# Performance work log

Hardware: AMD Instinct MI355X
Metric: run time of the kernel (lower is better)

The kernel has to match this reference:

```python
import jax, jax.numpy as jnp
import numpy as np

OBJ_THRESHOLD = 0.5  # matches module init kwarg
N, M, S = 128, 32, 512


def setup_inputs() -> dict:
    key = jax.random.key(0)
    k = jax.random.split(key, 6)
    # boxes are normalized cxcywh in [0,1]; keep them inside the image so
    # torch-style slice semantics (non-negative indices) are reproduced exactly
    p_cxy = jax.random.uniform(k[0], (N, M, 2), minval=0.3, maxval=0.7)
    p_wh = jax.random.uniform(k[1], (N, M, 2), minval=0.05, maxval=0.4)
    p_cls = jnp.zeros((N, M, 1), jnp.float32)  # C=1 -> all class 0
    p_obj = jax.random.uniform(k[2], (N, M, 1))
    pred_boxes = jnp.concatenate([p_cxy, p_wh, p_cls, p_obj], axis=-1)  # [N,M,6]
    t_cxy = jax.random.uniform(k[3], (N, M, 2), minval=0.3, maxval=0.7)
    t_wh = jax.random.uniform(k[4], (N, M, 2), minval=0.05, maxval=0.4)
    t_cls = jnp.zeros((N, M, 1), jnp.float32)
    target_boxes = jnp.concatenate([t_cxy, t_wh, t_cls], axis=-1)  # [N,M,5]
    return {"pred_boxes": pred_boxes, "target_boxes": target_boxes, "img_size": S}


def _rasterize(boxes, valid, img_size):
    # boxes: [N, M, >=4] normalized cxcywh; valid: [N, M] bool
    # Returns per-sample union-of-boxes mask [N, H, W] (C=1, cls ignored).
    b = img_size * jax.lax.stop_gradient(boxes[..., :4])
    cx, cy, w, h = b[..., 0], b[..., 1], b[..., 2], b[..., 3]
    # torch: .int() truncation (== trunc/floor for positive), then clamp_max(img_size)
    x1 = jnp.minimum((cx - w / 2).astype(jnp.int32), img_size)
    x2 = jnp.minimum((cx + w / 2).astype(jnp.int32), img_size)
    y1 = jnp.minimum((cy - h / 2).astype(jnp.int32), img_size)
    y2 = jnp.minimum((cy + h / 2).astype(jnp.int32), img_size)
    coords = jnp.arange(img_size, dtype=jnp.int32)
    ym = (coords >= y1[..., None]) & (coords < y2[..., None]) & valid[..., None]  # [N,M,H]
    xm = (coords >= x1[..., None]) & (coords < x2[..., None]) & valid[..., None]  # [N,M,W]
    # union over the M boxes without materializing [N,M,H,W]:
    cnt = jnp.einsum('nmh,nmw->nhw', ym.astype(jnp.float32), xm.astype(jnp.float32))
    return cnt > 0  # [N,H,W] bool


def reference(pred_boxes, target_boxes, img_size):
    pred_valid = pred_boxes[..., 5] > OBJ_THRESHOLD          # filter_obj_threshold
    tgt_valid = jnp.ones(target_boxes.shape[:2], dtype=bool)  # all targets valid
    m1 = _rasterize(pred_boxes, pred_valid, img_size)
    m2 = _rasterize(target_boxes, tgt_valid, img_size)
    intersection = (m1 & m2).astype(jnp.float32).sum()  # sum over (N,H,W), C=1
    union = (m1 | m2).astype(jnp.float32).sum()
    return intersection / jnp.maximum(union, 1.0)  # compute(): IoU scalar
```

## Files before the change

### kernel.cpp

```cpp
#include <hip/hip_runtime.h>


#define MAX_M 32
#define MAX_W 8

__global__ void box_mask_iou_kernel(const float* __restrict__ pred,
                                    const float* __restrict__ tgt,
                                    const int* __restrict__ img_size_p,
                                    unsigned int* __restrict__ counters,
                                    int M) {
    const int n   = blockIdx.x;
    const int S   = img_size_p[0];
    const int W   = (S + 63) >> 6;
    const int tid = threadIdx.x;

    __shared__ unsigned long long pmask[MAX_M][MAX_W];
    __shared__ unsigned long long tmask[MAX_M][MAX_W];
    __shared__ int py1[MAX_M], py2[MAX_M], ty1[MAX_M], ty2[MAX_M];

    if (tid < 2 * M) {
        const bool isPred = tid < M;
        const int  m      = isPred ? tid : tid - M;
        const float* b    = isPred ? (pred + (size_t)(n * M + m) * 6)
                                   : (tgt  + (size_t)(n * M + m) * 5);
        const float cx = (float)S * b[0];
        const float cy = (float)S * b[1];
        const float w  = (float)S * b[2];
        const float h  = (float)S * b[3];
        const bool valid = isPred ? (b[5] > 0.5f) : true;
        int x1 = min((int)(cx - w * 0.5f), S);
        int x2 = min((int)(cx + w * 0.5f), S);
        int y1 = min((int)(cy - h * 0.5f), S);
        int y2 = min((int)(cy + h * 0.5f), S);
        if (!valid) { x1 = 0; x2 = 0; y1 = 0; y2 = 0; }
        x1 = max(x1, 0);
        x2 = max(x2, 0);
        unsigned long long (*mask)[MAX_W] = isPred ? pmask : tmask;
        for (int j = 0; j < W; ++j) {
            const int lo = max(x1, j * 64);
            const int hi = min(x2, j * 64 + 64);
            unsigned long long mw = 0ull;
            if (hi > lo) {
                const int len = hi - lo;
                mw = (len >= 64) ? ~0ull : ((1ull << len) - 1ull);
                mw <<= (lo - j * 64);
            }
            mask[m][j] = mw;
        }
        if (isPred) { py1[m] = y1; py2[m] = y2; }
        else        { ty1[m] = y1; ty2[m] = y2; }
    }
    __syncthreads();

    unsigned int localI = 0, localU = 0;
    const int y = blockIdx.y * blockDim.x + tid;
    if (y < S) {
        unsigned long long pm[MAX_W], tm[MAX_W];
        #pragma unroll
        for (int j = 0; j < MAX_W; ++j) { pm[j] = 0ull; tm[j] = 0ull; }
        for (int m = 0; m < M; ++m) {
            if (y >= py1[m] && y < py2[m]) {
                for (int j = 0; j < W; ++j) pm[j] |= pmask[m][j];
            }
            if (y >= ty1[m] && y < ty2[m]) {
                for (int j = 0; j < W; ++j) tm[j] |= tmask[m][j];
            }
        }
        for (int j = 0; j < W; ++j) {
            localI += (unsigned int)__popcll(pm[j] & tm[j]);
            localU += (unsigned int)__popcll(pm[j] | tm[j]);
        }
    }

    #pragma unroll
    for (int off = 32; off > 0; off >>= 1) {
        localI += __shfl_down(localI, off);
        localU += __shfl_down(localU, off);
    }
    if ((tid & 63) == 0) {
        atomicAdd(&counters[0], localI);
        atomicAdd(&counters[1], localU);
    }
}

__global__ void finalize_kernel(const unsigned int* __restrict__ counters,
                                float* __restrict__ out) {
    const double I = (double)counters[0];
    const double U = (double)counters[1];
    out[0] = (float)(I / (U < 1.0 ? 1.0 : U));
}

extern "C" void kernel_launch(void* const* d_in, const int* in_sizes, int n_in,
                              void* d_out, int out_size, void* d_ws, size_t ws_size,
                              hipStream_t stream) {
    const float* pred  = (const float*)d_in[0];
    const float* tgt   = (const float*)d_in[1];
    const int*   imgsz = (const int*)d_in[2];
    float*       out   = (float*)d_out;

    const int M = 32;
    const int N = in_sizes[0] / (6 * M);

    unsigned int* counters = (unsigned int*)d_ws;
    hipMemsetAsync(counters, 0, 2 * sizeof(unsigned int), stream);

    dim3 grid(N, 2);
    box_mask_iou_kernel<<<grid, 256, 0, stream>>>(pred, tgt, imgsz, counters, M);
    finalize_kernel<<<1, 1, 0, stream>>>(counters, out);
}
```

Before: 41.08 us.

## Replace global atomics and memset with per-block partials and parallel finalize

Drops the memset and the global atomicAdd counters. Each block (one per sample, now 512 threads covering all rows) reduces its wave sums through shared memory and writes its own partial pair, and a 64-thread finalize kernel sums the partials with shuffles. This removes a memset launch, atomic contention and the duplicate per-sample box setup across two y-blocks. The cost is fewer blocks (128 instead of 256) and an extra shared-memory barrier.

```diff
diff --git a/kernel.cpp b/kernel.cpp
--- a/kernel.cpp
+++ b/kernel.cpp
@@ -1,28 +1,29 @@
 #include <hip/hip_runtime.h>
 
 
-#define MAX_M 32
+#define MBOX  32
 #define MAX_W 8
 
-__global__ void box_mask_iou_kernel(const float* __restrict__ pred,
-                                    const float* __restrict__ tgt,
-                                    const int* __restrict__ img_size_p,
-                                    unsigned int* __restrict__ counters,
-                                    int M) {
+__global__ __launch_bounds__(512)
+void box_mask_partial_kernel(const float* __restrict__ pred,
+                             const float* __restrict__ tgt,
+                             const int* __restrict__ img_size_p,
+                             unsigned int* __restrict__ partials) {
     const int n   = blockIdx.x;
     const int S   = img_size_p[0];
     const int W   = (S + 63) >> 6;
     const int tid = threadIdx.x;
 
-    __shared__ unsigned long long pmask[MAX_M][MAX_W];
-    __shared__ unsigned long long tmask[MAX_M][MAX_W];
-    __shared__ int py1[MAX_M], py2[MAX_M], ty1[MAX_M], ty2[MAX_M];
+    __shared__ unsigned long long pmask[MBOX][MAX_W];
+    __shared__ unsigned long long tmask[MBOX][MAX_W];
+    __shared__ int py1[MBOX], py2[MBOX], ty1[MBOX], ty2[MBOX];
+    __shared__ unsigned int waveI[8], waveU[8];
 
-    if (tid < 2 * M) {
-        const bool isPred = tid < M;
-        const int  m      = isPred ? tid : tid - M;
-        const float* b    = isPred ? (pred + (size_t)(n * M + m) * 6)
-                                   : (tgt  + (size_t)(n * M + m) * 5);
+    if (tid < 2 * MBOX) {
+        const bool isPred = tid < MBOX;
+        const int  m      = isPred ? tid : tid - MBOX;
+        const float* b    = isPred ? (pred + (size_t)(n * MBOX + m) * 6)
+                                   : (tgt  + (size_t)(n * MBOX + m) * 5);
         const float cx = (float)S * b[0];
         const float cy = (float)S * b[1];
         const float w  = (float)S * b[2];
@@ -53,12 +54,11 @@
     __syncthreads();
 
     unsigned int localI = 0, localU = 0;
-    const int y = blockIdx.y * blockDim.x + tid;
-    if (y < S) {
+    for (int y = tid; y < S; y += blockDim.x) {
         unsigned long long pm[MAX_W], tm[MAX_W];
         #pragma unroll
         for (int j = 0; j < MAX_W; ++j) { pm[j] = 0ull; tm[j] = 0ull; }
-        for (int m = 0; m < M; ++m) {
+        for (int m = 0; m < MBOX; ++m) {
             if (y >= py1[m] && y < py2[m]) {
                 for (int j = 0; j < W; ++j) pm[j] |= pmask[m][j];
             }
@@ -77,17 +77,35 @@
         localI += __shfl_down(localI, off);
         localU += __shfl_down(localU, off);
     }
-    if ((tid & 63) == 0) {
-        atomicAdd(&counters[0], localI);
-        atomicAdd(&counters[1], localU);
+    const int wave = tid >> 6;
+    if ((tid & 63) == 0) { waveI[wave] = localI; waveU[wave] = localU; }
+    __syncthreads();
+    if (tid == 0) {
+        unsigned int I = 0, U = 0;
+        const int nWaves = (int)(blockDim.x >> 6);
+        for (int wv = 0; wv < nWaves; ++wv) { I += waveI[wv]; U += waveU[wv]; }
+        partials[2 * n]     = I;
+        partials[2 * n + 1] = U;
     }
 }
 
-__global__ void finalize_kernel(const unsigned int* __restrict__ counters,
-                                float* __restrict__ out) {
-    const double I = (double)counters[0];
-    const double U = (double)counters[1];
-    out[0] = (float)(I / (U < 1.0 ? 1.0 : U));
+__global__ __launch_bounds__(64)
+void finalize_kernel(const unsigned int* __restrict__ partials,
+                     float* __restrict__ out, int nBlocks) {
+    unsigned int I = 0, U = 0;
+    for (int b = (int)threadIdx.x; b < nBlocks; b += 64) {
+        I += partials[2 * b];
+        U += partials[2 * b + 1];
+    }
+    #pragma unroll
+    for (int off = 32; off > 0; off >>= 1) {
+        I += __shfl_down(I, off);
+        U += __shfl_down(U, off);
+    }
+    if (threadIdx.x == 0) {
+        const double dU = (double)U;
+        out[0] = (float)((double)I / (dU < 1.0 ? 1.0 : dU));
+    }
 }
 
 extern "C" void kernel_launch(void* const* d_in, const int* in_sizes, int n_in,
@@ -98,13 +116,10 @@
     const int*   imgsz = (const int*)d_in[2];
     float*       out   = (float*)d_out;
 
-    const int M = 32;
-    const int N = in_sizes[0] / (6 * M);
+    const int N = in_sizes[0] / (6 * MBOX);
 
-    unsigned int* counters = (unsigned int*)d_ws;
-    hipMemsetAsync(counters, 0, 2 * sizeof(unsigned int), stream);
+    unsigned int* partials = (unsigned int*)d_ws;
 
-    dim3 grid(N, 2);
-    box_mask_iou_kernel<<<grid, 256, 0, stream>>>(pred, tgt, imgsz, counters, M);
-    finalize_kernel<<<1, 1, 0, stream>>>(counters, out);
+    box_mask_partial_kernel<<<N, 512, 0, stream>>>(pred, tgt, imgsz, partials);
+    finalize_kernel<<<1, 64, 0, stream>>>(partials, out, N);
 }
```

Result: faster. 34.60 us (-15.8%).
